# Kernel tuning notes

Hardware: AMD Instinct MI355X
Metric: run time of the kernel (lower is better)

Reference implementation:

```python
import jax, jax.numpy as jnp
import numpy as np

B, S, D, H = 4, 2048, 1024, 16
DH = D // H          # per-head attention size (attention_size // n_heads)
F = 4 * D            # FFN hidden
EPS = 1e-5


def _layer_norm(x, g, b):
    m = jnp.mean(x, axis=-1, keepdims=True)
    v = jnp.mean(jnp.square(x - m), axis=-1, keepdims=True)
    return (x - m) * jax.lax.rsqrt(v + EPS) * g + b


def setup_inputs() -> dict:
    key = jax.random.key(0)
    ks = jax.random.split(key, 12)
    s = 0.02
    x = jax.random.normal(ks[0], (B, S, D), dtype=jnp.float32)
    # causal mask: True = masked (strict upper triangle)
    mask = jnp.broadcast_to(jnp.triu(jnp.ones((S, S), dtype=bool), k=1), (B, S, S))
    wq = jax.random.normal(ks[1], (H, D, DH), dtype=jnp.float32) * s
    wk = jax.random.normal(ks[2], (H, D, DH), dtype=jnp.float32) * s
    wv = jax.random.normal(ks[3], (H, D, DH), dtype=jnp.float32) * s
    wo = jax.random.normal(ks[4], (D, D), dtype=jnp.float32) * s   # attention_size -> embedding_dim
    w1 = jax.random.normal(ks[5], (D, F), dtype=jnp.float32) * s
    b1 = jax.random.normal(ks[6], (F,), dtype=jnp.float32) * s
    w2 = jax.random.normal(ks[7], (F, D), dtype=jnp.float32) * s
    b2 = jax.random.normal(ks[8], (D,), dtype=jnp.float32) * s
    ln1_g = jnp.ones((D,), jnp.float32) + jax.random.normal(ks[9], (D,), jnp.float32) * s
    ln1_b = jax.random.normal(ks[10], (D,), jnp.float32) * s
    ln2_g = jnp.ones((D,), jnp.float32) + jax.random.normal(ks[11], (D,), jnp.float32) * s
    ln2_b = jnp.zeros((D,), jnp.float32)
    return {"x": x, "mask": mask, "wq": wq, "wk": wk, "wv": wv, "wo": wo,
            "w1": w1, "b1": b1, "w2": w2, "b2": b2,
            "ln1_g": ln1_g, "ln1_b": ln1_b, "ln2_g": ln2_g, "ln2_b": ln2_b}


def reference(x, mask, wq, wk, wv, wo, w1, b1, w2, b2, ln1_g, ln1_b, ln2_g, ln2_b):
    # --- self-attention block (pre-norm, residual) ---
    h = _layer_norm(x, ln1_g, ln1_b)                       # [B,S,D]
    q = jnp.einsum('bsd,hde->bhse', h, wq)                 # [B,H,S,DH]
    k = jnp.einsum('bsd,hde->bhse', h, wk)
    v = jnp.einsum('bsd,hde->bhse', h, wv)
    scores = jnp.einsum('bhse,bhte->bhst', q, k)           # [B,H,S,S]
    # faithful to source: mask-fill with -inf, THEN divide by sqrt(head_dim)
    scores = jnp.where(mask[:, None, :, :], -jnp.inf, scores) / jnp.sqrt(jnp.float32(DH))
    p = jax.nn.softmax(scores, axis=-1)
    attn = jnp.einsum('bhst,bhte->bhse', p, v)             # [B,H,S,DH]
    concat = attn.transpose(0, 2, 1, 3).reshape(B, S, D)   # heads concatenated on feature dim
    x = x + concat @ wo
    # --- feed-forward block ---
    h2 = _layer_norm(x, ln2_g, ln2_b)
    ff = jax.nn.gelu(h2 @ w1 + b1, approximate=False) @ w2 + b2
    return x + ff
```

## Files before the change

### kernel.cpp

```cpp
#include <hip/hip_runtime.h>
#include <hip/hip_bf16.h>
#include <math.h>


#define Bz 4
#define Sz 2048
#define Dz 1024
#define Hz 16
#define DHz 64
#define Fz 4096
#define Mz 8192

typedef float f32x4 __attribute__((ext_vector_type(4)));
typedef __bf16 bf16x8 __attribute__((ext_vector_type(8)));
typedef short s16x4 __attribute__((ext_vector_type(4)));

#define GLOAD_LDS16(g, l)                                                                   \
  __builtin_amdgcn_global_load_lds((const __attribute__((address_space(1))) unsigned int*)(g), \
                                   (__attribute__((address_space(3))) unsigned int*)(l), 16, 0, 0)

static __device__ __forceinline__ unsigned short f2bu(float f) {
  unsigned int u = __float_as_uint(f);
  u += 0x7fffu + ((u >> 16) & 1u);
  return (unsigned short)(u >> 16);
}

static __device__ __forceinline__ f32x4 mfma32(bf16x8 a, bf16x8 b, f32x4 c) {
  return __builtin_amdgcn_mfma_f32_16x16x32_bf16(a, b, c, 0, 0, 0);
}
static __device__ __forceinline__ f32x4 mfma16(s16x4 a, s16x4 b, f32x4 c) {
#if __has_builtin(__builtin_amdgcn_mfma_f32_16x16x16bf16_1k)
  return __builtin_amdgcn_mfma_f32_16x16x16bf16_1k(a, b, c, 0, 0, 0);
#else
  asm("v_mfma_f32_16x16x16_bf16 %0, %1, %2, %0" : "+v"(c) : "v"(a), "v"(b));
  return c;
#endif
}

template <int OFF>
static __device__ __forceinline__ s16x4 tr16(unsigned addr) {
  s16x4 r;
  asm volatile("ds_read_b64_tr_b16 %0, %1 offset:%2" : "=v"(r) : "v"(addr), "i"(OFF));
  return r;
}


__global__ __launch_bounds__(256) void pack_qkv(
    const float* __restrict__ wq, const float* __restrict__ wk, const float* __restrict__ wv,
    unsigned short* __restrict__ outW)
{
  int idx = blockIdx.x * 256 + threadIdx.x;
  int n = idx >> 10, d = idx & 1023;
  int proj = n >> 10, nn = n & 1023;
  int hh = nn >> 6, e = nn & 63;
  const float* w = proj == 0 ? wq : (proj == 1 ? wk : wv);
  outW[idx] = f2bu(w[((size_t)hh * Dz + d) * DHz + e]);
}

__global__ __launch_bounds__(256) void transpose_f32_to_bf16(
    const float* __restrict__ in, unsigned short* __restrict__ out, int R, int C)
{
  __shared__ float tile[32][33];
  int c0 = blockIdx.x * 32, r0 = blockIdx.y * 32;
  int x = threadIdx.x, y = threadIdx.y;
#pragma unroll
  for (int i = 0; i < 32; i += 8)
    tile[y + i][x] = in[(size_t)(r0 + y + i) * C + c0 + x];
  __syncthreads();
#pragma unroll
  for (int i = 0; i < 32; i += 8)
    out[(size_t)(c0 + y + i) * R + r0 + x] = f2bu(tile[x][y + i]);
}


__global__ __launch_bounds__(256) void ln_kernel(
    const float* __restrict__ x, const float* __restrict__ gamma, const float* __restrict__ beta,
    unsigned short* __restrict__ outH)
{
  const int row = blockIdx.x;
  const int tid = threadIdx.x;
  const float4 v = ((const float4*)(x + (size_t)row * Dz))[tid];
  float s = v.x + v.y + v.z + v.w;
  float s2 = v.x * v.x + v.y * v.y + v.z * v.z + v.w * v.w;
#pragma unroll
  for (int o = 32; o > 0; o >>= 1) {
    s += __shfl_xor(s, o);
    s2 += __shfl_xor(s2, o);
  }
  __shared__ float ss[4], ss2[4];
  if ((tid & 63) == 0) { ss[tid >> 6] = s; ss2[tid >> 6] = s2; }
  __syncthreads();
  s = ss[0] + ss[1] + ss[2] + ss[3];
  s2 = ss2[0] + ss2[1] + ss2[2] + ss2[3];
  const float mean = s * (1.0f / Dz);
  const float rstd = rsqrtf(s2 * (1.0f / Dz) - mean * mean + 1e-5f);
  const float4 g4 = ((const float4*)gamma)[tid];
  const float4 b4 = ((const float4*)beta)[tid];
  ushort4 o;
  o.x = f2bu((v.x - mean) * rstd * g4.x + b4.x);
  o.y = f2bu((v.y - mean) * rstd * g4.y + b4.y);
  o.z = f2bu((v.z - mean) * rstd * g4.z + b4.z);
  o.w = f2bu((v.w - mean) * rstd * g4.w + b4.w);
  ((ushort4*)(outH + (size_t)row * Dz))[tid] = o;
}


enum { EPI_BF16 = 0, EPI_GELU_BF16 = 1, EPI_RES_F32 = 2, EPI_BIAS_RES_F32 = 3 };

template <int EPI>
__global__ __launch_bounds__(256) void gemm_kernel(
    const unsigned short* __restrict__ A,
    const unsigned short* __restrict__ BT,
    int M, int N, int K,
    const float* bias, const float* resid,
    unsigned short* outb, float* outf)
{
  __shared__ unsigned short As[128 * 32];
  __shared__ unsigned short Bs[128 * 32];
  const int tid = threadIdx.x;
  const int lane = tid & 63;
  const int m0 = blockIdx.y * 128;
  const int n0 = blockIdx.x * 128;
  const int wm = ((tid >> 7) & 1) * 64;
  const int wn = ((tid >> 6) & 1) * 64;
  const int rsel = lane & 15;
  const int kgrp = lane >> 4;

  f32x4 acc[4][4] = {};

  const int kTiles = K >> 5;
  for (int kt = 0; kt < kTiles; ++kt) {
    if (kt) __syncthreads();
    const int kOff = kt * 32;
#pragma unroll
    for (int r = 0; r < 2; ++r) {
      int c = r * 256 + tid;
      int row = c >> 2;
      int kcs = (c & 3) ^ (row & 3);
      GLOAD_LDS16(A + (size_t)(m0 + row) * K + kOff + kcs * 8, &As[c * 8]);
      GLOAD_LDS16(BT + (size_t)(n0 + row) * K + kOff + kcs * 8, &Bs[c * 8]);
    }
    __syncthreads();
    bf16x8 af[4], bfr[4];
#pragma unroll
    for (int mf = 0; mf < 4; ++mf) {
      int row = wm + mf * 16 + rsel;
      af[mf] = *(const bf16x8*)&As[row * 32 + ((kgrp ^ (row & 3)) * 8)];
    }
#pragma unroll
    for (int nf = 0; nf < 4; ++nf) {
      int row = wn + nf * 16 + rsel;
      bfr[nf] = *(const bf16x8*)&Bs[row * 32 + ((kgrp ^ (row & 3)) * 8)];
    }
#pragma unroll
    for (int mf = 0; mf < 4; ++mf)
#pragma unroll
      for (int nf = 0; nf < 4; ++nf)
        acc[mf][nf] = mfma32(af[mf], bfr[nf], acc[mf][nf]);
  }

#pragma unroll
  for (int mf = 0; mf < 4; ++mf) {
#pragma unroll
    for (int nf = 0; nf < 4; ++nf) {
      const int n = n0 + wn + nf * 16 + rsel;
#pragma unroll
      for (int j = 0; j < 4; ++j) {
        const int m = m0 + wm + mf * 16 + kgrp * 4 + j;
        const size_t idx = (size_t)m * N + n;
        float v = acc[mf][nf][j];
        if constexpr (EPI == EPI_BF16) {
          outb[idx] = f2bu(v);
        } else if constexpr (EPI == EPI_GELU_BF16) {
          v += bias[n];
          v = 0.5f * v * (1.0f + erff(v * 0.70710678118654752f));
          outb[idx] = f2bu(v);
        } else if constexpr (EPI == EPI_RES_F32) {
          outf[idx] = v + resid[idx];
        } else {
          outf[idx] = v + bias[n] + resid[idx];
        }
      }
    }
  }
}


__global__ __launch_bounds__(256, 4) void attn_kernel(
    const unsigned short* __restrict__ QKV,
    unsigned short* __restrict__ outA)
{
  __shared__ unsigned short Kt[64 * 64];
  __shared__ unsigned short Vs[64 * 64];
  const int pi = blockIdx.x;
  const int hh = blockIdx.y;
  const int bb = blockIdx.z;
  const int tid = threadIdx.x;
  const int lane = tid & 63;
  const int w = tid >> 6;
  const int rsel = lane & 15;
  const int kgrp = lane >> 4;
  const int qtA = pi, qtB = 31 - pi;
  const int qgA = qtA * 64 + w * 16 + rsel;
  const int qgB = qtB * 64 + w * 16 + rsel;
  const size_t rowQA = (size_t)(bb * Sz + qgA) * 3072 + hh * 64;
  const size_t rowQB = (size_t)(bb * Sz + qgB) * 3072 + hh * 64;

  const bf16x8 qfA0 = *(const bf16x8*)&QKV[rowQA + kgrp * 8];
  const bf16x8 qfA1 = *(const bf16x8*)&QKV[rowQA + 32 + kgrp * 8];
  const bf16x8 qfB0 = *(const bf16x8*)&QKV[rowQB + kgrp * 8];
  const bf16x8 qfB1 = *(const bf16x8*)&QKV[rowQB + 32 + kgrp * 8];

  f32x4 accA[4] = {}, accB[4] = {};
  float mA = -INFINITY, lA = 0.0f, mB = -INFINITY, lB = 0.0f;

  auto vs3 = (__attribute__((address_space(3))) unsigned short*)Vs;
  const unsigned vbase = (unsigned)(uintptr_t)vs3 + (unsigned)lane * 8u;
  constexpr float SCL = 0.18033688011112042f;

  auto proc = [&](const bf16x8& qf0, const bf16x8& qf1, float& mrun, float& lrun,
                  f32x4* accO, s16x4* pb, bool edge, int qg, int kb) {
    f32x4 sc[4];
    __builtin_amdgcn_s_setprio(1);
#pragma unroll
    for (int kf = 0; kf < 4; ++kf) {
      int key = kf * 16 + rsel;
      bf16x8 k0 = *(const bf16x8*)&Kt[key * 64 + ((kgrp ^ (key & 7)) * 8)];
      bf16x8 k1 = *(const bf16x8*)&Kt[key * 64 + (((4 + kgrp) ^ (key & 7)) * 8)];
      f32x4 s = {};
      s = mfma32(k0, qf0, s);
      s = mfma32(k1, qf1, s);
      sc[kf] = s;
    }
    __builtin_amdgcn_s_setprio(0);
    float tmax = -INFINITY;
#pragma unroll
    for (int kf = 0; kf < 4; ++kf)
#pragma unroll
      for (int j = 0; j < 4; ++j) {
        float v = sc[kf][j] * SCL;
        if (edge) {
          int keyg = kb + kf * 16 + kgrp * 4 + j;
          if (keyg > qg) v = -INFINITY;
        }
        sc[kf][j] = v;
        tmax = fmaxf(tmax, v);
      }
    tmax = fmaxf(tmax, __shfl_xor(tmax, 16));
    tmax = fmaxf(tmax, __shfl_xor(tmax, 32));
    const float mnew = fmaxf(mrun, tmax);
    const float corr = exp2f(mrun - mnew);
    float psum = 0.0f;
#pragma unroll
    for (int kf = 0; kf < 4; ++kf) {
      s16x4 t;
#pragma unroll
      for (int j = 0; j < 4; ++j) {
        float e = exp2f(sc[kf][j] - mnew);
        psum += e;
        t[j] = (short)f2bu(e);
      }
      pb[kf] = t;
    }
    psum += __shfl_xor(psum, 16);
    psum += __shfl_xor(psum, 32);
    lrun = lrun * corr + psum;
    mrun = mnew;
#pragma unroll
    for (int df = 0; df < 4; ++df) accO[df] *= corr;
  };

  for (int kt = 0; kt <= qtB; ++kt) {
    const int kb = kt * 64;
    const bool doA = (kt <= qtA);
    if (kt) __syncthreads();
#pragma unroll
    for (int r = 0; r < 2; ++r) {
      int c = r * 256 + tid;
      int key = c >> 3;
      int dcs = (c & 7) ^ (key & 7);
      GLOAD_LDS16(QKV + (size_t)(bb * Sz + kb + key) * 3072 + 1024 + hh * 64 + dcs * 8,
                  &Kt[c * 8]);
    }
#pragma unroll
    for (int r = 0; r < 2; ++r) {
      int c = r * 256 + tid;
      int key = ((c >> 3) & 15) * 4 + ((c >> 1) & 3);
      int d = (c >> 7) * 16 + (c & 1) * 8;
      GLOAD_LDS16(QKV + (size_t)(bb * Sz + kb + key) * 3072 + 2048 + hh * 64 + d,
                  &Vs[c * 8]);
    }
    __syncthreads();

    s16x4 pbA[4], pbB[4];
    if (doA) proc(qfA0, qfA1, mA, lA, accA, pbA, kt == qtA, qgA, kb);
    proc(qfB0, qfB1, mB, lB, accB, pbB, kt == qtB, qgB, kb);

#pragma unroll
    for (int df = 0; df < 4; ++df) {
      unsigned a = vbase + df * 2048;
      s16x4 vf0 = tr16<0>(a);
      s16x4 vf1 = tr16<512>(a);
      s16x4 vf2 = tr16<1024>(a);
      s16x4 vf3 = tr16<1536>(a);
      asm volatile("s_waitcnt lgkmcnt(0)" ::: "memory");
      __builtin_amdgcn_sched_barrier(0);
      __builtin_amdgcn_s_setprio(1);
      if (doA) {
        accA[df] = mfma16(vf0, pbA[0], accA[df]);
        accA[df] = mfma16(vf1, pbA[1], accA[df]);
        accA[df] = mfma16(vf2, pbA[2], accA[df]);
        accA[df] = mfma16(vf3, pbA[3], accA[df]);
      }
      accB[df] = mfma16(vf0, pbB[0], accB[df]);
      accB[df] = mfma16(vf1, pbB[1], accB[df]);
      accB[df] = mfma16(vf2, pbB[2], accB[df]);
      accB[df] = mfma16(vf3, pbB[3], accB[df]);
      __builtin_amdgcn_s_setprio(0);
    }
  }

  auto epi = [&](const f32x4* accO, float lrun, int qg) {
    const float rl = 1.0f / lrun;
    const size_t orow = (size_t)(bb * Sz + qg) * Dz + hh * 64;
#pragma unroll
    for (int df = 0; df < 4; ++df) {
      s16x4 o;
#pragma unroll
      for (int j = 0; j < 4; ++j) o[j] = (short)f2bu(accO[df][j] * rl);
      *(s16x4*)&outA[orow + df * 16 + kgrp * 4] = o;
    }
  };
  epi(accA, lA, qgA);
  epi(accB, lB, qgB);
}


extern "C" void kernel_launch(void* const* d_in, const int* in_sizes, int n_in,
                              void* d_out, int out_size, void* d_ws, size_t ws_size,
                              hipStream_t stream) {
  const float* x   = (const float*)d_in[0];
  const float* wq  = (const float*)d_in[2];
  const float* wk  = (const float*)d_in[3];
  const float* wv  = (const float*)d_in[4];
  const float* wo  = (const float*)d_in[5];
  const float* w1  = (const float*)d_in[6];
  const float* b1  = (const float*)d_in[7];
  const float* w2  = (const float*)d_in[8];
  const float* b2  = (const float*)d_in[9];
  const float* g1  = (const float*)d_in[10];
  const float* be1 = (const float*)d_in[11];
  const float* g2  = (const float*)d_in[12];
  const float* be2 = (const float*)d_in[13];
  float* out = (float*)d_out;

  char* ws = (char*)d_ws;
  unsigned short* WqkvT = (unsigned short*)(ws);
  unsigned short* WoT   = (unsigned short*)(ws + 6291456);
  unsigned short* W1T   = (unsigned short*)(ws + 8388608);
  unsigned short* W2T   = (unsigned short*)(ws + 16777216);
  unsigned short* hbuf  = (unsigned short*)(ws + 25165824);
  unsigned short* big   = (unsigned short*)(ws + 41943040);

  dim3 tb(32, 8);
  pack_qkv<<<12288, 256, 0, stream>>>(wq, wk, wv, WqkvT);
  transpose_f32_to_bf16<<<dim3(32, 32), tb, 0, stream>>>(wo, WoT, 1024, 1024);
  transpose_f32_to_bf16<<<dim3(128, 32), tb, 0, stream>>>(w1, W1T, 1024, 4096);
  transpose_f32_to_bf16<<<dim3(32, 128), tb, 0, stream>>>(w2, W2T, 4096, 1024);

  ln_kernel<<<Mz, 256, 0, stream>>>(x, g1, be1, hbuf);
  gemm_kernel<EPI_BF16><<<dim3(24, 64), 256, 0, stream>>>(
      hbuf, WqkvT, Mz, 3072, 1024, nullptr, nullptr, big, nullptr);
  attn_kernel<<<dim3(16, 16, 4), 256, 0, stream>>>(big, hbuf);
  gemm_kernel<EPI_RES_F32><<<dim3(8, 64), 256, 0, stream>>>(
      hbuf, WoT, Mz, 1024, 1024, nullptr, x, nullptr, out);
  ln_kernel<<<Mz, 256, 0, stream>>>(out, g2, be2, hbuf);
  gemm_kernel<EPI_GELU_BF16><<<dim3(32, 64), 256, 0, stream>>>(
      hbuf, W1T, Mz, Fz, 1024, b1, nullptr, big, nullptr);
  gemm_kernel<EPI_BIAS_RES_F32><<<dim3(8, 64), 256, 0, stream>>>(
      big, W2T, Mz, 1024, Fz, b2, out, nullptr, out);
}
```

Before: 512.7 us.

## Double-buffer attention K/V tiles, remap blocks per XCD, lazy softmax rescale, tiled QKV pack

The attention kernel now double-buffers its K and V tiles in LDS, prefetching the next key tile with global_load_lds while the current one is computed, so load latency is hidden instead of stalling on a sync each iteration. Blocks are launched from a 1D grid and remapped so each XCD gets contiguous (batch, head) groups, which should improve L2 reuse of K/V. The online softmax skips the rescale of the accumulator unless the running max grows by more than 8 (log2 units), and bf16 conversion uses the native cast. Separately, the QKV weight pack becomes an LDS-tiled transpose with vectorized float4 loads and ushort4 stores, replacing uncoalesced strided reads. The cost is doubled LDS per block, which may lower occupancy, and a looser numeric bound on the exponentials.

```diff
diff --git a/kernel.cpp b/kernel.cpp
--- a/kernel.cpp
+++ b/kernel.cpp
@@ -13,6 +13,7 @@
 
 typedef float f32x4 __attribute__((ext_vector_type(4)));
 typedef __bf16 bf16x8 __attribute__((ext_vector_type(8)));
+typedef __bf16 bf16x4 __attribute__((ext_vector_type(4)));
 typedef short s16x4 __attribute__((ext_vector_type(4)));
 
 #define GLOAD_LDS16(g, l)                                                                   \
@@ -49,12 +50,33 @@
     const float* __restrict__ wq, const float* __restrict__ wk, const float* __restrict__ wv,
     unsigned short* __restrict__ outW)
 {
-  int idx = blockIdx.x * 256 + threadIdx.x;
-  int n = idx >> 10, d = idx & 1023;
-  int proj = n >> 10, nn = n & 1023;
-  int hh = nn >> 6, e = nn & 63;
-  const float* w = proj == 0 ? wq : (proj == 1 ? wk : wv);
-  outW[idx] = f2bu(w[((size_t)hh * Dz + d) * DHz + e]);
+  __shared__ float tile[64][65];
+  const int blk = blockIdx.x;
+  const int dc = blk & 15;
+  const int h  = (blk >> 4) & 15;
+  const int p  = blk >> 8;
+  const float* w = p == 0 ? wq : (p == 1 ? wk : wv);
+  const int tid = threadIdx.x;
+#pragma unroll
+  for (int i = 0; i < 4; ++i) {
+    int idx = i * 256 + tid;
+    int dl = idx >> 4;
+    int e0 = (idx & 15) * 4;
+    const float4 v = *(const float4*)&w[(size_t)(h * 1024 + dc * 64 + dl) * 64 + e0];
+    tile[dl][e0 + 0] = v.x; tile[dl][e0 + 1] = v.y;
+    tile[dl][e0 + 2] = v.z; tile[dl][e0 + 3] = v.w;
+  }
+  __syncthreads();
+#pragma unroll
+  for (int i = 0; i < 4; ++i) {
+    int idx = i * 256 + tid;
+    int e = idx >> 4;
+    int d0 = (idx & 15) * 4;
+    ushort4 o;
+    o.x = f2bu(tile[d0 + 0][e]); o.y = f2bu(tile[d0 + 1][e]);
+    o.z = f2bu(tile[d0 + 2][e]); o.w = f2bu(tile[d0 + 3][e]);
+    *(ushort4*)&outW[(size_t)(p * 1024 + h * 64 + e) * 1024 + dc * 64 + d0] = o;
+  }
 }
 
 __global__ __launch_bounds__(256) void transpose_f32_to_bf16(
@@ -190,11 +212,15 @@
     const unsigned short* __restrict__ QKV,
     unsigned short* __restrict__ outA)
 {
-  __shared__ unsigned short Kt[64 * 64];
-  __shared__ unsigned short Vs[64 * 64];
-  const int pi = blockIdx.x;
-  const int hh = blockIdx.y;
-  const int bb = blockIdx.z;
+  __shared__ unsigned short Kt[2][64 * 64];
+  __shared__ unsigned short Vs[2][64 * 64];
+  const int bid = blockIdx.x;
+  const int xcd = bid & 7;
+  const int t = bid >> 3;
+  const int pi = t & 15;
+  const int g = xcd * 8 + (t >> 4);
+  const int hh = g & 15;
+  const int bb = g >> 4;
   const int tid = threadIdx.x;
   const int lane = tid & 63;
   const int w = tid >> 6;
@@ -214,19 +240,39 @@
   f32x4 accA[4] = {}, accB[4] = {};
   float mA = -INFINITY, lA = 0.0f, mB = -INFINITY, lB = 0.0f;
 
-  auto vs3 = (__attribute__((address_space(3))) unsigned short*)Vs;
-  const unsigned vbase = (unsigned)(uintptr_t)vs3 + (unsigned)lane * 8u;
+  auto vs3 = (__attribute__((address_space(3))) unsigned short*)&Vs[0][0];
+  const unsigned vbase0 = (unsigned)(uintptr_t)vs3 + (unsigned)lane * 8u;
   constexpr float SCL = 0.18033688011112042f;
 
-  auto proc = [&](const bf16x8& qf0, const bf16x8& qf1, float& mrun, float& lrun,
-                  f32x4* accO, s16x4* pb, bool edge, int qg, int kb) {
+  auto stage = [&](int kt, int b) {
+    const int kb = kt * 64;
+#pragma unroll
+    for (int r = 0; r < 2; ++r) {
+      int c = r * 256 + tid;
+      int key = c >> 3;
+      int dcs = (c & 7) ^ (key & 7);
+      GLOAD_LDS16(QKV + (size_t)(bb * Sz + kb + key) * 3072 + 1024 + hh * 64 + dcs * 8,
+                  &Kt[b][c * 8]);
+    }
+#pragma unroll
+    for (int r = 0; r < 2; ++r) {
+      int c = r * 256 + tid;
+      int key = ((c >> 3) & 15) * 4 + ((c >> 1) & 3);
+      int d = (c >> 7) * 16 + (c & 1) * 8;
+      GLOAD_LDS16(QKV + (size_t)(bb * Sz + kb + key) * 3072 + 2048 + hh * 64 + d,
+                  &Vs[b][c * 8]);
+    }
+  };
+
+  auto proc = [&](const unsigned short* Kb, const bf16x8& qf0, const bf16x8& qf1,
+                  float& mrun, float& lrun, f32x4* accO, s16x4* pb, bool edge, int qg, int kb) {
     f32x4 sc[4];
     __builtin_amdgcn_s_setprio(1);
 #pragma unroll
     for (int kf = 0; kf < 4; ++kf) {
       int key = kf * 16 + rsel;
-      bf16x8 k0 = *(const bf16x8*)&Kt[key * 64 + ((kgrp ^ (key & 7)) * 8)];
-      bf16x8 k1 = *(const bf16x8*)&Kt[key * 64 + (((4 + kgrp) ^ (key & 7)) * 8)];
+      bf16x8 k0 = *(const bf16x8*)&Kb[key * 64 + ((kgrp ^ (key & 7)) * 8)];
+      bf16x8 k1 = *(const bf16x8*)&Kb[key * 64 + (((4 + kgrp) ^ (key & 7)) * 8)];
       f32x4 s = {};
       s = mfma32(k0, qf0, s);
       s = mfma32(k1, qf1, s);
@@ -248,57 +294,49 @@
       }
     tmax = fmaxf(tmax, __shfl_xor(tmax, 16));
     tmax = fmaxf(tmax, __shfl_xor(tmax, 32));
-    const float mnew = fmaxf(mrun, tmax);
-    const float corr = exp2f(mrun - mnew);
+    if (!__all(tmax <= mrun + 8.0f)) {
+      const float mnew = fmaxf(mrun, tmax);
+      const float corr = exp2f(mrun - mnew);
+      lrun *= corr;
+#pragma unroll
+      for (int df = 0; df < 4; ++df) accO[df] *= corr;
+      mrun = mnew;
+    }
     float psum = 0.0f;
 #pragma unroll
     for (int kf = 0; kf < 4; ++kf) {
-      s16x4 t;
+      bf16x4 pv;
 #pragma unroll
       for (int j = 0; j < 4; ++j) {
-        float e = exp2f(sc[kf][j] - mnew);
+        float e = exp2f(sc[kf][j] - mrun);
         psum += e;
-        t[j] = (short)f2bu(e);
+        pv[j] = (__bf16)e;
       }
-      pb[kf] = t;
+      pb[kf] = __builtin_bit_cast(s16x4, pv);
     }
     psum += __shfl_xor(psum, 16);
     psum += __shfl_xor(psum, 32);
-    lrun = lrun * corr + psum;
-    mrun = mnew;
-#pragma unroll
-    for (int df = 0; df < 4; ++df) accO[df] *= corr;
+    lrun += psum;
   };
+
+  stage(0, 0);
+  asm volatile("s_waitcnt vmcnt(0)" ::: "memory");
+  __syncthreads();
 
   for (int kt = 0; kt <= qtB; ++kt) {
     const int kb = kt * 64;
+    const int cur = kt & 1;
     const bool doA = (kt <= qtA);
-    if (kt) __syncthreads();
-#pragma unroll
-    for (int r = 0; r < 2; ++r) {
-      int c = r * 256 + tid;
-      int key = c >> 3;
-      int dcs = (c & 7) ^ (key & 7);
-      GLOAD_LDS16(QKV + (size_t)(bb * Sz + kb + key) * 3072 + 1024 + hh * 64 + dcs * 8,
-                  &Kt[c * 8]);
-    }
-#pragma unroll
-    for (int r = 0; r < 2; ++r) {
-      int c = r * 256 + tid;
-      int key = ((c >> 3) & 15) * 4 + ((c >> 1) & 3);
-      int d = (c >> 7) * 16 + (c & 1) * 8;
-      GLOAD_LDS16(QKV + (size_t)(bb * Sz + kb + key) * 3072 + 2048 + hh * 64 + d,
-                  &Vs[c * 8]);
-    }
-    __syncthreads();
+    if (kt < qtB) stage(kt + 1, cur ^ 1);
 
     s16x4 pbA[4], pbB[4];
-    if (doA) proc(qfA0, qfA1, mA, lA, accA, pbA, kt == qtA, qgA, kb);
-    proc(qfB0, qfB1, mB, lB, accB, pbB, kt == qtB, qgB, kb);
-
+    if (doA) proc(Kt[cur], qfA0, qfA1, mA, lA, accA, pbA, kt == qtA, qgA, kb);
+    proc(Kt[cur], qfB0, qfB1, mB, lB, accB, pbB, kt == qtB, qgB, kb);
+
+    const unsigned vb = vbase0 + (unsigned)cur * 8192u;
 #pragma unroll
     for (int df = 0; df < 4; ++df) {
-      unsigned a = vbase + df * 2048;
+      unsigned a = vb + df * 2048;
       s16x4 vf0 = tr16<0>(a);
       s16x4 vf1 = tr16<512>(a);
       s16x4 vf2 = tr16<1024>(a);
@@ -318,6 +356,11 @@
       accB[df] = mfma16(vf3, pbB[3], accB[df]);
       __builtin_amdgcn_s_setprio(0);
     }
+
+    if (kt < qtB) {
+      asm volatile("s_waitcnt vmcnt(0)" ::: "memory");
+      __syncthreads();
+    }
   }
 
   auto epi = [&](const f32x4* accO, float lrun, int qg) {
@@ -363,7 +406,7 @@
   unsigned short* big   = (unsigned short*)(ws + 41943040);
 
   dim3 tb(32, 8);
-  pack_qkv<<<12288, 256, 0, stream>>>(wq, wk, wv, WqkvT);
+  pack_qkv<<<768, 256, 0, stream>>>(wq, wk, wv, WqkvT);
   transpose_f32_to_bf16<<<dim3(32, 32), tb, 0, stream>>>(wo, WoT, 1024, 1024);
   transpose_f32_to_bf16<<<dim3(128, 32), tb, 0, stream>>>(w1, W1T, 1024, 4096);
   transpose_f32_to_bf16<<<dim3(32, 128), tb, 0, stream>>>(w2, W2T, 4096, 1024);
@@ -371,7 +414,7 @@
   ln_kernel<<<Mz, 256, 0, stream>>>(x, g1, be1, hbuf);
   gemm_kernel<EPI_BF16><<<dim3(24, 64), 256, 0, stream>>>(
       hbuf, WqkvT, Mz, 3072, 1024, nullptr, nullptr, big, nullptr);
-  attn_kernel<<<dim3(16, 16, 4), 256, 0, stream>>>(big, hbuf);
+  attn_kernel<<<1024, 256, 0, stream>>>(big, hbuf);
   gemm_kernel<EPI_RES_F32><<<dim3(8, 64), 256, 0, stream>>>(
       hbuf, WoT, Mz, 1024, 1024, nullptr, x, nullptr, out);
   ln_kernel<<<Mz, 256, 0, stream>>>(out, g2, be2, hbuf);
```

Result: slower. 547.9 us (+6.9%).
